# Performance work log

Measured on AMD Instinct MI355X. Metric: run time of the kernel, lower is better.

## Reference

```python
import jax, jax.numpy as jnp
import numpy as np

PADDING_VALUE = 0.0  # padding_value init arg


def setup_inputs() -> dict:
    key = jax.random.key(0)
    k1, k2 = jax.random.split(key)
    B, T, D = 16, 4096, 256
    x = jax.random.normal(k1, (B, T, D), dtype=jnp.float32)
    mask = jax.random.bernoulli(k2, 0.5, (B, T))  # bool
    return {"x": x, "mask": mask}


def reference(x, mask):
    # batch_first=True: x is [B, T, ...feat], mask is [B, T].
    B, T = mask.shape
    lens = mask.sum(axis=1)  # [B] number of selected elements per row
    # Stable argsort on (~mask) brings indices of True entries to the front,
    # preserving their original order -> index of the j-th True element.
    order = jnp.argsort(jnp.logical_not(mask), axis=1, stable=True)  # [B, T]
    # Gather x rows into compacted order.
    idx = order.reshape(order.shape + (1,) * (x.ndim - 2))  # [B, T, 1...]
    gathered = jnp.take_along_axis(x, idx, axis=1)  # [B, T, ...feat]
    # Right-pad positions j >= lens[b] with padding_value.
    valid = jnp.arange(T)[None, :] < lens[:, None]  # [B, T]
    valid = valid.reshape(valid.shape + (1,) * (x.ndim - 2))
    x_ = jnp.where(valid, gathered, jnp.asarray(PADDING_VALUE, x.dtype))
    return x_, lens
```

## Files before the change

### kernel.cpp

```cpp
#include <hip/hip_runtime.h>


#define BLK 256
#define ROWS 64

__global__ __launch_bounds__(BLK) void pad_masked_fused(
    const float* __restrict__ x,
    const int* __restrict__ mask,
    float* __restrict__ out,
    float* __restrict__ lens_f,
    int T, int D4) {

    const int c = blockIdx.x;
    const int b = blockIdx.y;
    const bool zeroPhase = (blockIdx.z != 0);
    const int tid = threadIdx.x;
    const int lane = tid & 63;
    const int wave = tid >> 6;

    const int* mrow = mask + (size_t)b * T;

    const int limit = zeroPhase ? T : c * ROWS;
    int partial = 0;
    for (int base = tid * 4; base < limit; base += BLK * 4) {
        const int4 mv = *reinterpret_cast<const int4*>(mrow + base);
        partial += (mv.x != 0) + (mv.y != 0) + (mv.z != 0) + (mv.w != 0);
    }
    __shared__ int wred[BLK / 64];
    int s = partial;
    #pragma unroll
    for (int off = 32; off; off >>= 1) s += __shfl_xor(s, off);
    if (lane == 0) wred[wave] = s;
    __syncthreads();
    const int P = wred[0] + wred[1] + wred[2] + wred[3];

    if (zeroPhase) {
        const int L = P;
        if (c == 0 && tid == 0) lens_f[b] = (float)L;
        const int j0 = c * ROWS;
        if (j0 + ROWS <= L) return;
        float4* orow = reinterpret_cast<float4*>(out) + ((size_t)b * T + j0) * (size_t)D4;
        const float4 z = make_float4(0.f, 0.f, 0.f, 0.f);
        for (int r = wave; r < ROWS; r += BLK / 64) {
            if (j0 + r >= L) {
                for (int t = lane; t < D4; t += 64)
                    orow[(size_t)r * D4 + t] = z;
            }
        }
        return;
    }

    __shared__ int selsh[ROWS];
    __shared__ int ranksh[ROWS];
    if (wave == 0) {
        const int m = (mrow[c * ROWS + lane] != 0);
        int incl = m;
        #pragma unroll
        for (int off = 1; off < 64; off <<= 1) {
            int v = __shfl_up(incl, off);
            if (lane >= off) incl += v;
        }
        selsh[lane] = m;
        ranksh[lane] = incl - m;
    }
    __syncthreads();

    const float4* xrow = reinterpret_cast<const float4*>(x) +
                         ((size_t)b * T + (size_t)c * ROWS) * (size_t)D4;
    float4* obase = reinterpret_cast<float4*>(out) + (size_t)b * T * (size_t)D4;
    for (int r = wave; r < ROWS; r += BLK / 64) {
        if (selsh[r]) {
            const size_t j = (size_t)(P + ranksh[r]);
            for (int t = lane; t < D4; t += 64)
                obase[j * D4 + t] = xrow[(size_t)r * D4 + t];
        }
    }
}

extern "C" void kernel_launch(void* const* d_in, const int* in_sizes, int n_in,
                              void* d_out, int out_size, void* d_ws, size_t ws_size,
                              hipStream_t stream) {
    const float* x = (const float*)d_in[0];
    const int* mask = (const int*)d_in[1];

    const int Nx = in_sizes[0];
    const int BT = in_sizes[1];
    const int B = out_size - Nx;
    const int T = BT / B;
    const int D = Nx / BT;
    const int D4 = D / 4;

    float* out = (float*)d_out;
    float* lens_f = out + (size_t)Nx;

    dim3 grid(T / ROWS, B, 2);
    pad_masked_fused<<<grid, BLK, 0, stream>>>(x, mask, out, lens_f, T, D4);
}
```

Baseline: 22.23 us.

## Merge copy and zero-fill phases into one block, compact selected rows list

Drops the second grid z-phase. Each block now computes both the prefix count and the total row length in one packed 64-bit reduction, then copies its selected rows and zero-fills its own tail range. Selected rows are compacted into a list, so waves iterate only over valid rows and process two rows per iteration for more loads in flight. This halves the block count and removes a second full mask scan, at the cost of every block scanning the entire mask row.

```diff
diff --git a/kernel.cpp b/kernel.cpp
--- a/kernel.cpp
+++ b/kernel.cpp
@@ -2,6 +2,7 @@
 
 
 #define BLK 256
+#define NW (BLK / 64)
 #define ROWS 64
 
 __global__ __launch_bounds__(BLK) void pad_masked_fused(
@@ -13,67 +14,83 @@
 
     const int c = blockIdx.x;
     const int b = blockIdx.y;
-    const bool zeroPhase = (blockIdx.z != 0);
     const int tid = threadIdx.x;
     const int lane = tid & 63;
     const int wave = tid >> 6;
+    const int j0 = c * ROWS;
 
     const int* mrow = mask + (size_t)b * T;
 
-    const int limit = zeroPhase ? T : c * ROWS;
-    int partial = 0;
-    for (int base = tid * 4; base < limit; base += BLK * 4) {
-        const int4 mv = *reinterpret_cast<const int4*>(mrow + base);
-        partial += (mv.x != 0) + (mv.y != 0) + (mv.z != 0) + (mv.w != 0);
+    int pre = 0, all = 0;
+    for (int e = tid * 4; e < T; e += BLK * 4) {
+        const int4 mv = *reinterpret_cast<const int4*>(mrow + e);
+        const int t0 = (mv.x != 0), t1 = (mv.y != 0), t2 = (mv.z != 0), t3 = (mv.w != 0);
+        all += t0 + t1 + t2 + t3;
+        if (e + 3 < j0) {
+            pre += t0 + t1 + t2 + t3;
+        } else if (e < j0) {
+            pre += t0;
+            pre += (e + 1 < j0) ? t1 : 0;
+            pre += (e + 2 < j0) ? t2 : 0;
+            pre += (e + 3 < j0) ? t3 : 0;
+        }
     }
-    __shared__ int wred[BLK / 64];
-    int s = partial;
+    unsigned long long packed =
+        (unsigned long long)pre | ((unsigned long long)all << 32);
     #pragma unroll
-    for (int off = 32; off; off >>= 1) s += __shfl_xor(s, off);
-    if (lane == 0) wred[wave] = s;
+    for (int off = 32; off; off >>= 1) packed += __shfl_xor(packed, off);
+
+    __shared__ unsigned long long wred[NW];
+    __shared__ int selRows[ROWS];
+    __shared__ int nsel;
+    if (lane == 0) wred[wave] = packed;
     __syncthreads();
-    const int P = wred[0] + wred[1] + wred[2] + wred[3];
 
-    if (zeroPhase) {
-        const int L = P;
-        if (c == 0 && tid == 0) lens_f[b] = (float)L;
-        const int j0 = c * ROWS;
-        if (j0 + ROWS <= L) return;
-        float4* orow = reinterpret_cast<float4*>(out) + ((size_t)b * T + j0) * (size_t)D4;
-        const float4 z = make_float4(0.f, 0.f, 0.f, 0.f);
-        for (int r = wave; r < ROWS; r += BLK / 64) {
-            if (j0 + r >= L) {
-                for (int t = lane; t < D4; t += 64)
-                    orow[(size_t)r * D4 + t] = z;
-            }
-        }
-        return;
-    }
+    unsigned long long tot = 0;
+    #pragma unroll
+    for (int w = 0; w < NW; ++w) tot += wred[w];
+    const int P = (int)(tot & 0xffffffffull);
+    const int L = (int)(tot >> 32);
 
-    __shared__ int selsh[ROWS];
-    __shared__ int ranksh[ROWS];
     if (wave == 0) {
-        const int m = (mrow[c * ROWS + lane] != 0);
+        const int m = (mrow[j0 + lane] != 0);
         int incl = m;
         #pragma unroll
         for (int off = 1; off < 64; off <<= 1) {
-            int v = __shfl_up(incl, off);
+            const int v = __shfl_up(incl, off);
             if (lane >= off) incl += v;
         }
-        selsh[lane] = m;
-        ranksh[lane] = incl - m;
+        if (m) selRows[incl - 1] = lane;
+        if (lane == 63) nsel = incl;
     }
     __syncthreads();
+    const int n = nsel;
+
+    if (c == 0 && tid == 0) lens_f[b] = (float)L;
 
     const float4* xrow = reinterpret_cast<const float4*>(x) +
-                         ((size_t)b * T + (size_t)c * ROWS) * (size_t)D4;
+                         ((size_t)b * T + j0) * (size_t)D4;
     float4* obase = reinterpret_cast<float4*>(out) + (size_t)b * T * (size_t)D4;
-    for (int r = wave; r < ROWS; r += BLK / 64) {
-        if (selsh[r]) {
-            const size_t j = (size_t)(P + ranksh[r]);
-            for (int t = lane; t < D4; t += 64)
-                obase[j * D4 + t] = xrow[(size_t)r * D4 + t];
+    const float4 z = make_float4(0.f, 0.f, 0.f, 0.f);
+
+    for (int i = wave; i < n; i += 2 * NW) {
+        const int i2 = i + NW;
+        const bool h2 = (i2 < n);
+        const int r0 = selRows[i];
+        const int r1 = h2 ? selRows[i2] : 0;
+        for (int t = lane; t < D4; t += 64) {
+            const float4 v0 = xrow[(size_t)r0 * D4 + t];
+            float4 v1 = z;
+            if (h2) v1 = xrow[(size_t)r1 * D4 + t];
+            obase[(size_t)(P + i) * D4 + t] = v0;
+            if (h2) obase[(size_t)(P + i2) * D4 + t] = v1;
         }
+    }
+
+    const int zstart = (L > j0) ? L : j0;
+    for (int j = zstart + wave; j < j0 + ROWS; j += NW) {
+        for (int t = lane; t < D4; t += 64)
+            obase[(size_t)j * D4 + t] = z;
     }
 }
 
@@ -93,6 +110,6 @@
     float* out = (float*)d_out;
     float* lens_f = out + (size_t)Nx;
 
-    dim3 grid(T / ROWS, B, 2);
+    dim3 grid(T / ROWS, B);
     pad_masked_fused<<<grid, BLK, 0, stream>>>(x, mask, out, lens_f, T, D4);
 }
```

New measurement: 22.61 us. About the same (+1.7%).
